# Optimization experiments

Measured on AMD Instinct MI355X. Metric: run time of the kernel, lower is better.

The kernel has to match this reference:

```python
import jax, jax.numpy as jnp
import numpy as np

B, BS, M, D = 64, 8, 512, 256  # b = bs * neg_sample_num, neg_sample_num = 8
NEG_FILL = -1e10


def setup_inputs() -> dict:
    key = jax.random.key(0)
    ks = jax.random.split(key, 7)
    x = jax.random.normal(ks[0], (B, M, D), jnp.float32)
    y = jax.random.normal(ks[1], (BS, M, D), jnp.float32)
    mask_x = jax.random.randint(ks[2], (B, M), 0, 2).astype(bool).at[:, 0].set(True)
    mask_y = jax.random.randint(ks[3], (BS, M), 0, 2).astype(bool).at[:, 0].set(True)
    scale = 1.0 / np.sqrt(D)
    Wq = jax.random.normal(ks[4], (D, D), jnp.float32) * scale  # torch Linear weight [out,in]
    Wk = jax.random.normal(ks[5], (D, D), jnp.float32) * scale
    Wv = jax.random.normal(ks[6], (D, D), jnp.float32) * scale
    return {"x": x, "y": y, "mask_x": mask_x, "mask_y": mask_y, "Wq": Wq, "Wk": Wk, "Wv": Wv}


def reference(x, y, mask_x, mask_y, Wq, Wk, Wv):
    # Projections (torch Linear: x @ W.T, no bias)
    Qx, Kx, Vx = x @ Wq.T, x @ Wk.T, x @ Wv.T
    Qy, Ky, Vy = y @ Wq.T, y @ Wk.T, y @ Wv.T
    b, m, d = Qx.shape
    bs = Ky.shape[0]
    neg = b // bs  # neg_sample_num branch (bs != b)

    scores_x = jnp.einsum('bid,bjd->bij', Qx, Kx)   # [b,m,m]
    scores_y = jnp.einsum('bid,bjd->bij', Qy, Ky)   # [bs,m,m]
    # Q_x grouped as [bs, neg, m, d] then transposed to [neg, bs, m, d];
    # K_y is tiled over neg (pure broadcast), so contract directly against [bs,m,d].
    Qx_e = Qx.reshape(bs, neg, m, d).swapaxes(0, 1)  # [neg,bs,m,d]
    scores_xy = jnp.einsum('nsid,sjd->nsij', Qx_e, Ky)  # [neg,bs,m,m]

    mx = mask_x[:, :, None]  # [b,m,1]
    my = mask_y[:, :, None]  # [bs,m,1]
    scores_x = jnp.where(mx & mx.swapaxes(1, 2), scores_x, NEG_FILL)
    scores_y = jnp.where(my & my.swapaxes(1, 2), scores_y, NEG_FILL)

    mask_xy = mask_x.reshape(bs, neg, m, 1).swapaxes(0, 1) & mask_y[None, :, None, :]  # [neg,bs,m,m]
    scores_xy = jnp.where(mask_xy, scores_xy, NEG_FILL)

    # y_len[n, s] = sum(mask_y[s]) for every n (repeat/view/sum/transpose in torch)
    y_len = jnp.broadcast_to(jnp.sum(mask_y.astype(jnp.int32), axis=1)[None, :], (neg, bs))

    probs_x = jax.nn.softmax(scores_x, axis=-1)
    probs_y = jax.nn.softmax(scores_y, axis=-1)
    probs_xy = jax.nn.softmax(scores_xy, axis=-1)

    ctx_x = jnp.einsum('bij,bjd->bid', probs_x, Vx)
    ctx_y = jnp.einsum('bij,bjd->bid', probs_y, Vy)
    return (ctx_x, ctx_y, scores_x, scores_y, probs_xy, mask_xy, y_len)
```

## Files before the change

kernel.cpp:

```cpp
#include <hip/hip_runtime.h>
#include <cstdint>

#define NEG_FILL_F (-10000000000.0f)
constexpr int BB     = 64;
constexpr int BS_    = 8;
constexpr int MM     = 512;
constexpr int DD     = 256;
constexpr int ROWS_X = BB * MM;
constexpr int ROWS_Y = BS_ * MM;
constexpr int ROWS_ALL = ROWS_X + ROWS_Y;
constexpr int KS     = 512;

typedef __attribute__((ext_vector_type(8))) short short8;
typedef __attribute__((ext_vector_type(4))) float f32x4;

__device__ inline unsigned short rne_bf16(float f) {
    unsigned int u = __float_as_uint(f);
    u = (u + 0x7FFFu + ((u >> 16) & 1u)) >> 16;
    return (unsigned short)u;
}
__device__ inline float bf2f(unsigned short h) {
    return __uint_as_float(((unsigned int)h) << 16);
}

__device__ inline f32x4 mfma16(short8 a, short8 b, f32x4 c) {
    return __builtin_amdgcn_mfma_f32_16x16x32_bf16(a, b, c, 0, 0, 0);
}

__device__ inline void gld16(const unsigned short* g, unsigned short* l) {
    __builtin_amdgcn_global_load_lds(
        (const __attribute__((address_space(1))) unsigned int*)g,
        (__attribute__((address_space(3))) unsigned int*)l, 16, 0, 0);
}

__device__ inline void mfma_4x4(const short8 af[4], const short8 bf_[4],
                                f32x4 acc[4][4]) {
    #pragma unroll
    for (int i = 0; i < 4; ++i)
        #pragma unroll
        for (int j = 0; j < 4; ++j)
            acc[i][j] = mfma16(af[i], bf_[j], acc[i][j]);
}

template<bool ASIDE>
__device__ inline void stage_qk(unsigned short* dstbase,
                                const unsigned short* __restrict__ src,
                                int ck, int wave, int lane)
{
    #pragma unroll
    for (int s = 0; s < 6; ++s) {
        const int c  = s * 256 + wave * 64 + lane;
        const int r  = c / 12;
        const int q  = c - r * 12;
        const int rm = r % 12;
        int cin = q - rm;
        cin += (cin >> 31) & 12;
        const int slotb = ck * 96 + cin * 8;
        const int p  = slotb >> 8;
        const int c8 = slotb & 255;
        const int off = ASIDE ? ((p == 1) ? 256 : 0)
                              : ((p == 2) ? 256 : 0);
        gld16(src + (size_t)r * KS + off + c8,
              dstbase + (size_t)(s * 256 + wave * 64) * 8);
    }
}

__device__ inline void frag4_rot96(const unsigned short (*T)[96], int rbase,
                                   int lid, const int rm[4], int c0,
                                   short8 f[4])
{
    #pragma unroll
    for (int i = 0; i < 4; ++i) {
        int q = c0 + rm[i];
        if (q >= 12) q -= 12;
        f[i] = *(const short8*)&T[rbase + i * 16 + lid][q * 8];
    }
}

__global__ __launch_bounds__(256) void convw_kernel(
    const float* __restrict__ Wq, const float* __restrict__ Wk,
    const float* __restrict__ Wv, unsigned short* __restrict__ Wb)
{
    const int g  = blockIdx.x * 256 + threadIdx.x;
    const int e  = g * 8;
    const int zi = e >> 16;
    const int off = e & 65535;
    const int row = off >> 8, k0 = off & 255;
    const float* W = (zi == 0) ? Wq : (zi == 1 ? Wk : Wv);
    float4 v0 = *(const float4*)(W + off);
    float4 v1 = *(const float4*)(W + off + 4);
    const float fv[8] = {v0.x, v0.y, v0.z, v0.w, v1.x, v1.y, v1.z, v1.w};
    short8 hh, ll;
    #pragma unroll
    for (int i = 0; i < 8; ++i) {
        unsigned short h = rne_bf16(fv[i]);
        hh[i] = (short)h;
        ll[i] = (short)rne_bf16(fv[i] - bf2f(h));
    }
    unsigned short* dst = Wb + (size_t)zi * 131072 + (size_t)row * KS;
    *(short8*)(dst + k0)       = hh;
    *(short8*)(dst + 256 + k0) = ll;
}

__global__ __launch_bounds__(256) void proj_kernel(
    const float* __restrict__ x, const float* __restrict__ y,
    const unsigned short* __restrict__ Wb,
    unsigned short* __restrict__ Qa, unsigned short* __restrict__ Kb,
    unsigned short* __restrict__ Vt)
{
    const int z    = blockIdx.z;
    const int row0 = blockIdx.x * 128;
    const int col0 = blockIdx.y * 128;
    const float* A = (row0 < ROWS_X) ? (x + (size_t)row0 * DD)
                                     : (y + (size_t)(row0 - ROWS_X) * DD);
    const unsigned short* Bsrc = Wb + (size_t)z * 131072 + (size_t)col0 * KS;

    __shared__ unsigned short Ab[128][96];
    __shared__ unsigned short Bb[128][96];

    const int t = threadIdx.x;
    const int wave = t >> 6, lane = t & 63, quad = lane >> 4, lid = lane & 15;
    const int wrow = (wave & 1) * 64, wcol = (wave >> 1) * 64;

    int rma[4], rmb[4];
    #pragma unroll
    for (int i = 0; i < 4; ++i) {
        rma[i] = (wrow + i * 16 + lid) % 12;
        rmb[i] = (wcol + i * 16 + lid) % 12;
    }

    f32x4 acc[4][4];
    #pragma unroll
    for (int i = 0; i < 4; ++i)
        #pragma unroll
        for (int j = 0; j < 4; ++j) acc[i][j] = (f32x4){0.f, 0.f, 0.f, 0.f};

    for (int ck = 0; ck < 8; ++ck) {
        stage_qk<false>(&Bb[0][0], Bsrc, ck, wave, lane);
        #pragma unroll
        for (int s = 0; s < 6; ++s) {
            const int c  = s * 256 + t;
            const int r  = c / 12;
            const int q  = c - r * 12;
            const int rm = r % 12;
            int cin = q - rm;
            cin += (cin >> 31) & 12;
            const int slotb = ck * 96 + cin * 8;
            const int p  = slotb >> 8;
            const int c8 = slotb & 255;
            const float* ap = A + (size_t)r * DD + c8;
            float4 v0 = *(const float4*)ap;
            float4 v1 = *(const float4*)(ap + 4);
            const float fv[8] = {v0.x, v0.y, v0.z, v0.w, v1.x, v1.y, v1.z, v1.w};
            short8 o;
            if (p == 1) {
                #pragma unroll
                for (int e = 0; e < 8; ++e) {
                    unsigned short h = rne_bf16(fv[e]);
                    o[e] = (short)rne_bf16(fv[e] - bf2f(h));
                }
            } else {
                #pragma unroll
                for (int e = 0; e < 8; ++e) o[e] = (short)rne_bf16(fv[e]);
            }
            *(short8*)&Ab[r][q * 8] = o;
        }
        __syncthreads();
        #pragma unroll
        for (int kk = 0; kk < 96; kk += 32) {
            const int c0 = (kk >> 3) + quad;
            short8 af[4], bf_[4];
            frag4_rot96(Ab, wrow, lid, rma, c0, af);
            frag4_rot96(Bb, wcol, lid, rmb, c0, bf_);
            mfma_4x4(af, bf_, acc);
        }
        __syncthreads();
    }

    if (z == 2) {
        #pragma unroll
        for (int i = 0; i < 4; ++i) {
            const int rg = row0 + wrow + i * 16 + quad * 4;
            const int b  = rg >> 9;
            const int j  = rg & 511;
            #pragma unroll
            for (int jt = 0; jt < 4; ++jt) {
                const int col = col0 + wcol + jt * 16 + lid;
                *(ushort4*)(Vt + (size_t)b * DD * MM + (size_t)col * MM + j) =
                    make_ushort4(rne_bf16(acc[i][jt][0]), rne_bf16(acc[i][jt][1]),
                                 rne_bf16(acc[i][jt][2]), rne_bf16(acc[i][jt][3]));
            }
        }
    } else {
        unsigned short* dst = (z == 0) ? Qa : Kb;
        #pragma unroll
        for (int i = 0; i < 4; ++i) {
            const int rg = row0 + wrow + i * 16 + quad * 4;
            #pragma unroll
            for (int r = 0; r < 4; ++r) {
                unsigned short* rowp = dst + (size_t)(rg + r) * KS;
                #pragma unroll
                for (int jt = 0; jt < 4; ++jt) {
                    const int col = col0 + wcol + jt * 16 + lid;
                    const float v = acc[i][jt][r];
                    unsigned short h = rne_bf16(v);
                    rowp[col]       = h;
                    rowp[256 + col] = rne_bf16(v - bf2f(h));
                }
            }
        }
    }
}

__global__ __launch_bounds__(256) void scores_self_kernel(
    const unsigned short* __restrict__ Qa,
    const unsigned short* __restrict__ Kb,
    const int* __restrict__ mask_x, const int* __restrict__ mask_y,
    float* __restrict__ Sbase, float2* __restrict__ pstats)
{
    const int z    = blockIdx.z;
    const int row0 = blockIdx.x * 128;
    const int col0 = blockIdx.y * 128;
    const unsigned short* Asrc = Qa + (size_t)(z * MM + row0) * KS;
    const unsigned short* Bsrc = Kb + (size_t)(z * MM + col0) * KS;
    const int* msk = (z < 64) ? (mask_x + z * MM) : (mask_y + (z - 64) * MM);
    float* S = Sbase + (size_t)z * MM * MM;

    __shared__ unsigned short Ab[128][96];
    __shared__ unsigned short Bb[128][96];
    __shared__ float pm2[128][2];
    __shared__ float ps2[128][2];

    const int t = threadIdx.x;
    const int wave = t >> 6, lane = t & 63, quad = lane >> 4, lid = lane & 15;
    const int wrow = (wave & 1) * 64, wcol = (wave >> 1) * 64;

    int rma[4], rmb[4];
    #pragma unroll
    for (int i = 0; i < 4; ++i) {
        rma[i] = (wrow + i * 16 + lid) % 12;
        rmb[i] = (wcol + i * 16 + lid) % 12;
    }

    f32x4 acc[4][4];
    #pragma unroll
    for (int i = 0; i < 4; ++i)
        #pragma unroll
        for (int j = 0; j < 4; ++j) acc[i][j] = (f32x4){0.f, 0.f, 0.f, 0.f};

    for (int ck = 0; ck < 8; ++ck) {
        stage_qk<true >(&Ab[0][0], Asrc, ck, wave, lane);
        stage_qk<false>(&Bb[0][0], Bsrc, ck, wave, lane);
        __syncthreads();
        #pragma unroll
        for (int kk = 0; kk < 96; kk += 32) {
            const int c0 = (kk >> 3) + quad;
            short8 af[4], bf_[4];
            frag4_rot96(Ab, wrow, lid, rma, c0, af);
            frag4_rot96(Bb, wcol, lid, rmb, c0, bf_);
            mfma_4x4(af, bf_, acc);
        }
        __syncthreads();
    }

    int mcol[4];
    #pragma unroll
    for (int jt = 0; jt < 4; ++jt) mcol[jt] = msk[col0 + wcol + jt * 16 + lid];

    #pragma unroll
    for (int i = 0; i < 4; ++i) {
        const int rl0 = wrow + i * 16 + quad * 4;
        #pragma unroll
        for (int r = 0; r < 4; ++r) {
            const int rlocal = rl0 + r;
            const int rg = row0 + rlocal;
            const bool mr = (msk[rg] != 0);
            float* Srow = S + (size_t)rg * MM;
            float v[4];
            float mt = -3.4e38f;
            #pragma unroll
            for (int jt = 0; jt < 4; ++jt) {
                const int col = col0 + wcol + jt * 16 + lid;
                const bool valid = mr && (mcol[jt] != 0);
                v[jt] = valid ? acc[i][jt][r] : NEG_FILL_F;
                Srow[col] = v[jt];
                mt = fmaxf(mt, v[jt]);
            }
            #pragma unroll
            for (int o = 1; o < 16; o <<= 1) mt = fmaxf(mt, __shfl_xor(mt, o));
            float se = 0.f;
            #pragma unroll
            for (int jt = 0; jt < 4; ++jt) se += __expf(v[jt] - mt);
            #pragma unroll
            for (int o = 1; o < 16; o <<= 1) se += __shfl_xor(se, o);
            if (lid == 0) { pm2[rlocal][wave >> 1] = mt; ps2[rlocal][wave >> 1] = se; }
        }
    }
    __syncthreads();
    if (t < 128) {
        const float m0 = pm2[t][0], m1 = pm2[t][1];
        const float mm = fmaxf(m0, m1);
        const float ss = ps2[t][0] * __expf(m0 - mm) + ps2[t][1] * __expf(m1 - mm);
        pstats[(size_t)(z * 4 + blockIdx.y) * MM + row0 + t] = make_float2(mm, ss);
    }
}

__global__ __launch_bounds__(256) void scores_xy_kernel(
    const unsigned short* __restrict__ Qa, const unsigned short* __restrict__ Kb,
    const int* __restrict__ mask_x, const int* __restrict__ mask_y,
    float* __restrict__ Sbase, float* __restrict__ Mbase,
    float2* __restrict__ pstats)
{
    const int z = blockIdx.z;
    const int n = z >> 3, s = z & 7;
    const int bq = s * 8 + n;
    const int bk = s;
    const int row0 = blockIdx.x * 128;
    const int col0 = blockIdx.y * 128;
    const unsigned short* Asrc = Qa + (size_t)(bq * MM + row0) * KS;
    const unsigned short* Bsrc = Kb + (size_t)((ROWS_X + bk * MM) + col0) * KS;
    const int* mq = mask_x + bq * MM;
    const int* mk = mask_y + bk * MM;
    float* Sl = Sbase + (size_t)z * MM * MM;
    float* Ml = Mbase + (size_t)z * MM * MM;

    __shared__ unsigned short Ab[128][64];
    __shared__ unsigned short Bb[128][64];
    __shared__ float pm2[128][2];
    __shared__ float ps2[128][2];

    const int t = threadIdx.x;
    const int wave = t >> 6, lane = t & 63, quad = lane >> 4, lid = lane & 15;
    const int wrow = (wave & 1) * 64, wcol = (wave >> 1) * 64;
    const int x7 = lid & 7;

    f32x4 acc[4][4];
    #pragma unroll
    for (int i = 0; i < 4; ++i)
        #pragma unroll
        for (int j = 0; j < 4; ++j) acc[i][j] = (f32x4){0.f, 0.f, 0.f, 0.f};

    for (int ck = 0; ck < 4; ++ck) {
        #pragma unroll
        for (int s4 = 0; s4 < 4; ++s4) {
            const int c   = s4 * 256 + wave * 64 + lane;
            const int r   = c >> 3;
            const int cin = (c & 7) ^ (r & 7);
            gld16(Asrc + (size_t)r * KS + ck * 64 + cin * 8,
                  &Ab[0][0] + (size_t)(s4 * 256 + wave * 64) * 8);
        }
        #pragma unroll
        for (int s4 = 0; s4 < 4; ++s4) {
            const int c   = s4 * 256 + wave * 64 + lane;
            const int r   = c >> 3;
            const int cin = (c & 7) ^ (r & 7);
            gld16(Bsrc + (size_t)r * KS + ck * 64 + cin * 8,
                  &Bb[0][0] + (size_t)(s4 * 256 + wave * 64) * 8);
        }
        __syncthreads();
        #pragma unroll
        for (int kk = 0; kk < 64; kk += 32) {
            const int c0 = (kk >> 3) + quad;
            const int q  = c0 ^ x7;
            short8 af[4], bf_[4];
            #pragma unroll
            for (int i = 0; i < 4; ++i) {
                af[i]  = *(const short8*)&Ab[wrow + i * 16 + lid][q * 8];
                bf_[i] = *(const short8*)&Bb[wcol + i * 16 + lid][q * 8];
            }
            mfma_4x4(af, bf_, acc);
        }
        __syncthreads();
    }

    int mcol[4];
    #pragma unroll
    for (int jt = 0; jt < 4; ++jt) mcol[jt] = mk[col0 + wcol + jt * 16 + lid];

    #pragma unroll
    for (int i = 0; i < 4; ++i) {
        const int rl0 = wrow + i * 16 + quad * 4;
        #pragma unroll
        for (int r = 0; r < 4; ++r) {
            const int rlocal = rl0 + r;
            const int rg = row0 + rlocal;
            const bool mr = (mq[rg] != 0);
            float* Srow = Sl + (size_t)rg * MM;
            float* Mrow = Ml + (size_t)rg * MM;
            float v[4];
            float mt = -3.4e38f;
            #pragma unroll
            for (int jt = 0; jt < 4; ++jt) {
                const int col = col0 + wcol + jt * 16 + lid;
                const bool valid = mr && (mcol[jt] != 0);
                v[jt] = valid ? acc[i][jt][r] : NEG_FILL_F;
                Srow[col] = v[jt];
                Mrow[col] = valid ? 1.0f : 0.0f;
                mt = fmaxf(mt, v[jt]);
            }
            #pragma unroll
            for (int o = 1; o < 16; o <<= 1) mt = fmaxf(mt, __shfl_xor(mt, o));
            float se = 0.f;
            #pragma unroll
            for (int jt = 0; jt < 4; ++jt) se += __expf(v[jt] - mt);
            #pragma unroll
            for (int o = 1; o < 16; o <<= 1) se += __shfl_xor(se, o);
            if (lid == 0) { pm2[rlocal][wave >> 1] = mt; ps2[rlocal][wave >> 1] = se; }
        }
    }
    __syncthreads();
    if (t < 128) {
        const float m0 = pm2[t][0], m1 = pm2[t][1];
        const float mm = fmaxf(m0, m1);
        const float ss = ps2[t][0] * __expf(m0 - mm) + ps2[t][1] * __expf(m1 - mm);
        pstats[(size_t)(z * 4 + blockIdx.y) * MM + row0 + t] = make_float2(mm, ss);
    }
}

__global__ __launch_bounds__(256) void reduce4_kernel(
    const float2* __restrict__ p, float2* __restrict__ st)
{
    const int row = blockIdx.x * 256 + threadIdx.x;
    const int z = row >> 9, rl = row & 511;
    float m = -3.4e38f, s = 0.f;
    #pragma unroll
    for (int by = 0; by < 4; ++by) {
        float2 v = p[(size_t)(z * 4 + by) * MM + rl];
        float nm = fmaxf(m, v.x);
        s = s * __expf(m - nm) + v.y * __expf(v.x - nm);
        m = nm;
    }
    st[row] = make_float2(m, 1.0f / s);
}

__global__ __launch_bounds__(256) void ctx_kernel(
    const float* __restrict__ Sbase, const float2* __restrict__ stats,
    const unsigned short* __restrict__ Vt_base, float* __restrict__ Obase)
{
    const int b = blockIdx.z;
    const float*          S  = Sbase + (size_t)b * MM * MM;
    const float2*         st = stats + (size_t)b * MM;
    const unsigned short* Vt = Vt_base + (size_t)b * DD * MM;
    float*                O  = Obase + (size_t)b * MM * DD;

    const int row0 = blockIdx.x * 128;
    const int col0 = blockIdx.y * 128;

    __shared__ unsigned short Ab[128][64];
    __shared__ unsigned short Bb[128][64];

    const int t = threadIdx.x;
    const int wave = t >> 6, lane = t & 63, quad = lane >> 4, lid = lane & 15;
    const int wrow = (wave & 1) * 64, wcol = (wave >> 1) * 64;
    const int x7 = lid & 7;

    f32x4 acc[4][4];
    #pragma unroll
    for (int i = 0; i < 4; ++i)
        #pragma unroll
        for (int j = 0; j < 4; ++j) acc[i][j] = (f32x4){0.f, 0.f, 0.f, 0.f};

    for (int ck = 0; ck < 8; ++ck) {
        #pragma unroll
        for (int s4 = 0; s4 < 4; ++s4) {
            const int c   = s4 * 256 + wave * 64 + lane;
            const int r   = c >> 3;
            const int cin = (c & 7) ^ (r & 7);
            gld16(Vt + (size_t)(col0 + r) * MM + ck * 64 + cin * 8,
                  &Bb[0][0] + (size_t)(s4 * 256 + wave * 64) * 8);
        }
        #pragma unroll
        for (int s4 = 0; s4 < 4; ++s4) {
            const int c    = s4 * 256 + t;
            const int row  = c >> 3;
            const int j8   = (c & 7) * 8;
            const int slot = (c & 7) ^ (row & 7);
            const float* sp = S + (size_t)(row0 + row) * MM + ck * 64 + j8;
            float4 v0 = *(const float4*)sp;
            float4 v1 = *(const float4*)(sp + 4);
            const float pm = st[row0 + row].x;
            short8 pk;
            pk[0] = (short)rne_bf16(__expf(v0.x - pm));
            pk[1] = (short)rne_bf16(__expf(v0.y - pm));
            pk[2] = (short)rne_bf16(__expf(v0.z - pm));
            pk[3] = (short)rne_bf16(__expf(v0.w - pm));
            pk[4] = (short)rne_bf16(__expf(v1.x - pm));
            pk[5] = (short)rne_bf16(__expf(v1.y - pm));
            pk[6] = (short)rne_bf16(__expf(v1.z - pm));
            pk[7] = (short)rne_bf16(__expf(v1.w - pm));
            *(short8*)&Ab[row][slot * 8] = pk;
        }
        __syncthreads();
        #pragma unroll
        for (int kk = 0; kk < 64; kk += 32) {
            const int c0 = (kk >> 3) + quad;
            const int q  = c0 ^ x7;
            short8 af[4], bf_[4];
            #pragma unroll
            for (int i = 0; i < 4; ++i) {
                af[i]  = *(const short8*)&Ab[wrow + i * 16 + lid][q * 8];
                bf_[i] = *(const short8*)&Bb[wcol + i * 16 + lid][q * 8];
            }
            mfma_4x4(af, bf_, acc);
        }
        __syncthreads();
    }

    #pragma unroll
    for (int i = 0; i < 4; ++i) {
        const int rgb = row0 + wrow + i * 16 + quad * 4;
        float inv[4];
        #pragma unroll
        for (int r = 0; r < 4; ++r) inv[r] = st[rgb + r].y;
        #pragma unroll
        for (int jt = 0; jt < 4; ++jt) {
            const int col = col0 + wcol + jt * 16 + lid;
            #pragma unroll
            for (int r = 0; r < 4; ++r)
                O[(size_t)(rgb + r) * DD + col] = acc[i][jt][r] * inv[r];
        }
    }
}

__global__ __launch_bounds__(128) void softmax_apply(
    float* __restrict__ S, const float2* __restrict__ stats)
{
    const int row = blockIdx.x;
    const float2 st = stats[row];
    float4* r = (float4*)(S + (size_t)row * MM) + threadIdx.x;
    float4 v = *r;
    v.x = __expf(v.x - st.x) * st.y;
    v.y = __expf(v.y - st.x) * st.y;
    v.z = __expf(v.z - st.x) * st.y;
    v.w = __expf(v.w - st.x) * st.y;
    *r = v;
}

__global__ void ylen_kernel(const int* __restrict__ mask_y, float* __restrict__ out)
{
    const int s = blockIdx.x;
    const int lane = threadIdx.x;
    int c = 0;
    #pragma unroll
    for (int k = 0; k < 8; ++k) c += (mask_y[s * MM + k * 64 + lane] != 0);
    #pragma unroll
    for (int off = 32; off; off >>= 1) c += __shfl_xor(c, off);
    if (lane < 8) out[lane * 8 + s] = (float)c;
}

extern "C" void kernel_launch(void* const* d_in, const int* in_sizes, int n_in,
                              void* d_out, int out_size, void* d_ws, size_t ws_size,
                              hipStream_t stream)
{
    const float* x      = (const float*)d_in[0];
    const float* y      = (const float*)d_in[1];
    const int*   mask_x = (const int*)d_in[2];
    const int*   mask_y = (const int*)d_in[3];
    const float* Wq     = (const float*)d_in[4];
    const float* Wk     = (const float*)d_in[5];
    const float* Wv     = (const float*)d_in[6];
    float* out = (float*)d_out;

    unsigned short* Wb = (unsigned short*)d_ws;
    unsigned short* Qa = Wb + 393216;
    unsigned short* Kb = Qa + 18874368;
    unsigned short* Vt = Kb + 18874368;
    float2* stats_x  = (float2*)(Vt + 9437184);
    float2* stats_xy = stats_x + ROWS_ALL;
    float2* ps_x  = stats_x + (ROWS_ALL + ROWS_X);
    float2* ps_xy = ps_x + (64 + 8) * 4 * 512;

    float* out_ctx_x = out;
    float* out_sx    = out + 9437184;
    float* out_pxy   = out + 28311552;
    float* out_mxy   = out + 45088768;
    float* out_ylen  = out + 61865984;

    convw_kernel<<<96, 256, 0, stream>>>(Wq, Wk, Wv, Wb);
    ylen_kernel<<<8, 64, 0, stream>>>(mask_y, out_ylen);

    proj_kernel<<<dim3(288, 2, 3), 256, 0, stream>>>(x, y, Wb, Qa, Kb, Vt);

    scores_self_kernel<<<dim3(4, 4, 72), 256, 0, stream>>>(
        Qa, Kb, mask_x, mask_y, out_sx, ps_x);
    scores_xy_kernel<<<dim3(4, 4, 64), 256, 0, stream>>>(
        Qa, Kb, mask_x, mask_y, out_pxy, out_mxy, ps_xy);

    reduce4_kernel<<<(ROWS_ALL + ROWS_X) / 256, 256, 0, stream>>>(ps_x, stats_x);

    softmax_apply<<<ROWS_X, 128, 0, stream>>>(out_pxy, stats_xy);

    ctx_kernel<<<dim3(4, 2, 72), 256, 0, stream>>>(out_sx, stats_x, Vt, out_ctx_x);
}
```

Baseline: 567.6 us.

## Pre-split x/y into bf16 hi/lo buffer and use 64-wide XOR-swizzled LDS staging

```diff
diff --git a/kernel.cpp b/kernel.cpp
--- a/kernel.cpp
+++ b/kernel.cpp
@@ -42,39 +42,30 @@
             acc[i][j] = mfma16(af[i], bf_[j], acc[i][j]);
 }
 
-template<bool ASIDE>
-__device__ inline void stage_qk(unsigned short* dstbase,
-                                const unsigned short* __restrict__ src,
-                                int ck, int wave, int lane)
-{
-    #pragma unroll
-    for (int s = 0; s < 6; ++s) {
-        const int c  = s * 256 + wave * 64 + lane;
-        const int r  = c / 12;
-        const int q  = c - r * 12;
-        const int rm = r % 12;
-        int cin = q - rm;
-        cin += (cin >> 31) & 12;
-        const int slotb = ck * 96 + cin * 8;
-        const int p  = slotb >> 8;
-        const int c8 = slotb & 255;
-        const int off = ASIDE ? ((p == 1) ? 256 : 0)
-                              : ((p == 2) ? 256 : 0);
-        gld16(src + (size_t)r * KS + off + c8,
-              dstbase + (size_t)(s * 256 + wave * 64) * 8);
-    }
-}
-
-__device__ inline void frag4_rot96(const unsigned short (*T)[96], int rbase,
-                                   int lid, const int rm[4], int c0,
-                                   short8 f[4])
-{
-    #pragma unroll
-    for (int i = 0; i < 4; ++i) {
-        int q = c0 + rm[i];
-        if (q >= 12) q -= 12;
+__device__ inline int awin(int w) { return ((((w >> 2) == 1) ? 256 : 0) + (w & 3) * 64); }
+__device__ inline int bwin(int w) { return ((((w >> 2) == 2) ? 256 : 0) + (w & 3) * 64); }
+
+__device__ inline void stage64(unsigned short* dstbase,
+                               const unsigned short* __restrict__ src,
+                               int srccol, int wave, int lane)
+{
+    #pragma unroll
+    for (int s4 = 0; s4 < 4; ++s4) {
+        const int c   = s4 * 256 + wave * 64 + lane;
+        const int r   = c >> 3;
+        const int cin = (c & 7) ^ (r & 7);
+        gld16(src + (size_t)r * KS + srccol + cin * 8,
+              dstbase + (size_t)(s4 * 256 + wave * 64) * 8);
+    }
+}
+
+__device__ inline void frag4_x64(const unsigned short (*T)[64], int rbase,
+                                 int lid, int c0, short8 f[4])
+{
+    const int q = c0 ^ (lid & 7);
+    #pragma unroll
+    for (int i = 0; i < 4; ++i)
         f[i] = *(const short8*)&T[rbase + i * 16 + lid][q * 8];
-    }
 }
 
 __global__ __launch_bounds__(256) void convw_kernel(
@@ -102,8 +93,32 @@
     *(short8*)(dst + 256 + k0) = ll;
 }
 
+__global__ __launch_bounds__(256) void convx_kernel(
+    const float* __restrict__ x, const float* __restrict__ y,
+    unsigned short* __restrict__ xs)
+{
+    const int g   = blockIdx.x * 256 + threadIdx.x;
+    const int row = g >> 5;
+    const int off = (g & 31) * 8;
+    const float* src = (row < ROWS_X) ? (x + (size_t)row * DD)
+                                      : (y + (size_t)(row - ROWS_X) * DD);
+    float4 v0 = *(const float4*)(src + off);
+    float4 v1 = *(const float4*)(src + off + 4);
+    const float fv[8] = {v0.x, v0.y, v0.z, v0.w, v1.x, v1.y, v1.z, v1.w};
+    short8 hh, ll;
+    #pragma unroll
+    for (int i = 0; i < 8; ++i) {
+        unsigned short h = rne_bf16(fv[i]);
+        hh[i] = (short)h;
+        ll[i] = (short)rne_bf16(fv[i] - bf2f(h));
+    }
+    unsigned short* dst = xs + (size_t)row * KS;
+    *(short8*)(dst + off)       = hh;
+    *(short8*)(dst + 256 + off) = ll;
+}
+
 __global__ __launch_bounds__(256) void proj_kernel(
-    const float* __restrict__ x, const float* __restrict__ y,
+    const unsigned short* __restrict__ xs,
     const unsigned short* __restrict__ Wb,
     unsigned short* __restrict__ Qa, unsigned short* __restrict__ Kb,
     unsigned short* __restrict__ Vt)
@@ -111,67 +126,32 @@
     const int z    = blockIdx.z;
     const int row0 = blockIdx.x * 128;
     const int col0 = blockIdx.y * 128;
-    const float* A = (row0 < ROWS_X) ? (x + (size_t)row0 * DD)
-                                     : (y + (size_t)(row0 - ROWS_X) * DD);
+    const unsigned short* Asrc = xs + (size_t)row0 * KS;
     const unsigned short* Bsrc = Wb + (size_t)z * 131072 + (size_t)col0 * KS;
 
-    __shared__ unsigned short Ab[128][96];
-    __shared__ unsigned short Bb[128][96];
+    __shared__ unsigned short Ab[128][64];
+    __shared__ unsigned short Bb[128][64];
 
     const int t = threadIdx.x;
     const int wave = t >> 6, lane = t & 63, quad = lane >> 4, lid = lane & 15;
     const int wrow = (wave & 1) * 64, wcol = (wave >> 1) * 64;
 
-    int rma[4], rmb[4];
-    #pragma unroll
-    for (int i = 0; i < 4; ++i) {
-        rma[i] = (wrow + i * 16 + lid) % 12;
-        rmb[i] = (wcol + i * 16 + lid) % 12;
-    }
-
     f32x4 acc[4][4];
     #pragma unroll
     for (int i = 0; i < 4; ++i)
         #pragma unroll
         for (int j = 0; j < 4; ++j) acc[i][j] = (f32x4){0.f, 0.f, 0.f, 0.f};
 
-    for (int ck = 0; ck < 8; ++ck) {
-        stage_qk<false>(&Bb[0][0], Bsrc, ck, wave, lane);
-        #pragma unroll
-        for (int s = 0; s < 6; ++s) {
-            const int c  = s * 256 + t;
-            const int r  = c / 12;
-            const int q  = c - r * 12;
-            const int rm = r % 12;
-            int cin = q - rm;
-            cin += (cin >> 31) & 12;
-            const int slotb = ck * 96 + cin * 8;
-            const int p  = slotb >> 8;
-            const int c8 = slotb & 255;
-            const float* ap = A + (size_t)r * DD + c8;
-            float4 v0 = *(const float4*)ap;
-            float4 v1 = *(const float4*)(ap + 4);
-            const float fv[8] = {v0.x, v0.y, v0.z, v0.w, v1.x, v1.y, v1.z, v1.w};
-            short8 o;
-            if (p == 1) {
-                #pragma unroll
-                for (int e = 0; e < 8; ++e) {
-                    unsigned short h = rne_bf16(fv[e]);
-                    o[e] = (short)rne_bf16(fv[e] - bf2f(h));
-                }
-            } else {
-                #pragma unroll
-                for (int e = 0; e < 8; ++e) o[e] = (short)rne_bf16(fv[e]);
-            }
-            *(short8*)&Ab[r][q * 8] = o;
-        }
-        __syncthreads();
-        #pragma unroll
-        for (int kk = 0; kk < 96; kk += 32) {
+    for (int w = 0; w < 12; ++w) {
+        stage64(&Ab[0][0], Asrc, awin(w), wave, lane);
+        stage64(&Bb[0][0], Bsrc, bwin(w), wave, lane);
+        __syncthreads();
+        #pragma unroll
+        for (int kk = 0; kk < 64; kk += 32) {
             const int c0 = (kk >> 3) + quad;
             short8 af[4], bf_[4];
-            frag4_rot96(Ab, wrow, lid, rma, c0, af);
-            frag4_rot96(Bb, wcol, lid, rmb, c0, bf_);
+            frag4_x64(Ab, wrow, lid, c0, af);
+            frag4_x64(Bb, wcol, lid, c0, bf_);
             mfma_4x4(af, bf_, acc);
         }
         __syncthreads();
@@ -226,8 +206,8 @@
     const int* msk = (z < 64) ? (mask_x + z * MM) : (mask_y + (z - 64) * MM);
     float* S = Sbase + (size_t)z * MM * MM;
 
-    __shared__ unsigned short Ab[128][96];
-    __shared__ unsigned short Bb[128][96];
+    __shared__ unsigned short Ab[128][64];
+    __shared__ unsigned short Bb[128][64];
     __shared__ float pm2[128][2];
     __shared__ float ps2[128][2];
 
@@ -235,29 +215,22 @@
     const int wave = t >> 6, lane = t & 63, quad = lane >> 4, lid = lane & 15;
     const int wrow = (wave & 1) * 64, wcol = (wave >> 1) * 64;
 
-    int rma[4], rmb[4];
-    #pragma unroll
-    for (int i = 0; i < 4; ++i) {
-        rma[i] = (wrow + i * 16 + lid) % 12;
-        rmb[i] = (wcol + i * 16 + lid) % 12;
-    }
-
     f32x4 acc[4][4];
     #pragma unroll
     for (int i = 0; i < 4; ++i)
         #pragma unroll
         for (int j = 0; j < 4; ++j) acc[i][j] = (f32x4){0.f, 0.f, 0.f, 0.f};
 
-    for (int ck = 0; ck < 8; ++ck) {
-        stage_qk<true >(&Ab[0][0], Asrc, ck, wave, lane);
-        stage_qk<false>(&Bb[0][0], Bsrc, ck, wave, lane);
-        __syncthreads();
-        #pragma unroll
-        for (int kk = 0; kk < 96; kk += 32) {
+    for (int w = 0; w < 12; ++w) {
+        stage64(&Ab[0][0], Asrc, awin(w), wave, lane);
+        stage64(&Bb[0][0], Bsrc, bwin(w), wave, lane);
+        __syncthreads();
+        #pragma unroll
+        for (int kk = 0; kk < 64; kk += 32) {
             const int c0 = (kk >> 3) + quad;
             short8 af[4], bf_[4];
-            frag4_rot96(Ab, wrow, lid, rma, c0, af);
-            frag4_rot96(Bb, wcol, lid, rmb, c0, bf_);
+            frag4_x64(Ab, wrow, lid, c0, af);
+            frag4_x64(Bb, wcol, lid, c0, bf_);
             mfma_4x4(af, bf_, acc);
         }
         __syncthreads();
@@ -332,7 +305,6 @@
     const int t = threadIdx.x;
     const int wave = t >> 6, lane = t & 63, quad = lane >> 4, lid = lane & 15;
     const int wrow = (wave & 1) * 64, wcol = (wave >> 1) * 64;
-    const int x7 = lid & 7;
 
     f32x4 acc[4][4];
     #pragma unroll
@@ -341,33 +313,15 @@
         for (int j = 0; j < 4; ++j) acc[i][j] = (f32x4){0.f, 0.f, 0.f, 0.f};
 
     for (int ck = 0; ck < 4; ++ck) {
-        #pragma unroll
-        for (int s4 = 0; s4 < 4; ++s4) {
-            const int c   = s4 * 256 + wave * 64 + lane;
-            const int r   = c >> 3;
-            const int cin = (c & 7) ^ (r & 7);
-            gld16(Asrc + (size_t)r * KS + ck * 64 + cin * 8,
-                  &Ab[0][0] + (size_t)(s4 * 256 + wave * 64) * 8);
-        }
-        #pragma unroll
-        for (int s4 = 0; s4 < 4; ++s4) {
-            const int c   = s4 * 256 + wave * 64 + lane;
-            const int r   = c >> 3;
-            const int cin = (c & 7) ^ (r & 7);
-            gld16(Bsrc + (size_t)r * KS + ck * 64 + cin * 8,
-                  &Bb[0][0] + (size_t)(s4 * 256 + wave * 64) * 8);
-        }
+        stage64(&Ab[0][0], Asrc, ck * 64, wave, lane);
+        stage64(&Bb[0][0], Bsrc, ck * 64, wave, lane);
         __syncthreads();
         #pragma unroll
         for (int kk = 0; kk < 64; kk += 32) {
             const int c0 = (kk >> 3) + quad;
-            const int q  = c0 ^ x7;
             short8 af[4], bf_[4];
-            #pragma unroll
-            for (int i = 0; i < 4; ++i) {
-                af[i]  = *(const short8*)&Ab[wrow + i * 16 + lid][q * 8];
-                bf_[i] = *(const short8*)&Bb[wcol + i * 16 + lid][q * 8];
-            }
+            frag4_x64(Ab, wrow, lid, c0, af);
+            frag4_x64(Bb, wcol, lid, c0, bf_);
             mfma_4x4(af, bf_, acc);
         }
         __syncthreads();
@@ -452,7 +406,6 @@
     const int t = threadIdx.x;
     const int wave = t >> 6, lane = t & 63, quad = lane >> 4, lid = lane & 15;
     const int wrow = (wave & 1) * 64, wcol = (wave >> 1) * 64;
-    const int x7 = lid & 7;
 
     f32x4 acc[4][4];
     #pragma unroll
@@ -494,13 +447,9 @@
         #pragma unroll
         for (int kk = 0; kk < 64; kk += 32) {
             const int c0 = (kk >> 3) + quad;
-            const int q  = c0 ^ x7;
             short8 af[4], bf_[4];
-            #pragma unroll
-            for (int i = 0; i < 4; ++i) {
-                af[i]  = *(const short8*)&Ab[wrow + i * 16 + lid][q * 8];
-                bf_[i] = *(const short8*)&Bb[wcol + i * 16 + lid][q * 8];
-            }
+            frag4_x64(Ab, wrow, lid, c0, af);
+            frag4_x64(Bb, wcol, lid, c0, bf_);
             mfma_4x4(af, bf_, acc);
         }
         __syncthreads();
@@ -562,7 +511,8 @@
     float* out = (float*)d_out;
 
     unsigned short* Wb = (unsigned short*)d_ws;
-    unsigned short* Qa = Wb + 393216;
+    unsigned short* xs = Wb + 393216;
+    unsigned short* Qa = xs + 18874368;
     unsigned short* Kb = Qa + 18874368;
     unsigned short* Vt = Kb + 18874368;
     float2* stats_x  = (float2*)(Vt + 9437184);
@@ -577,9 +527,10 @@
     float* out_ylen  = out + 61865984;
 
     convw_kernel<<<96, 256, 0, stream>>>(Wq, Wk, Wv, Wb);
+    convx_kernel<<<4608, 256, 0, stream>>>(x, y, xs);
     ylen_kernel<<<8, 64, 0, stream>>>(mask_y, out_ylen);
 
-    proj_kernel<<<dim3(288, 2, 3), 256, 0, stream>>>(x, y, Wb, Qa, Kb, Vt);
+    proj_kernel<<<dim3(288, 2, 3), 256, 0, stream>>>(xs, Wb, Qa, Kb, Vt);
 
     scores_self_kernel<<<dim3(4, 4, 72), 256, 0, stream>>>(
         Qa, Kb, mask_x, mask_y, out_sx, ps_x);
```

Measured after the change: 516.8 us. -8.9%, faster.
